# Kernel optimization log

Measured on AMD Instinct MI355X. Metric: run time of the kernel, lower is better.

Reference implementation:

```python
import jax, jax.numpy as jnp
import numpy as np

# SRM neuron constants (match init_kwargs)
THRESH = 0.3
TAU_M = 16.0
TAU_S = 4.0
DT = 1.0
LENS = 0.5
DECAY_M = float(np.exp(-DT / TAU_M))
DECAY_S = float(np.exp(-DT / TAU_S))

B, T = 16, 16
SHAPES = [(B, 64, 64, 64), (B, 128, 64, 64), (B, 128, 32, 32), (B, 512), (B, 11)]


@jax.custom_vjp
def spike_fn(u):
    # Heaviside spike with rectangular surrogate gradient (width 2*lens),
    # the smooth-math stand-in for the LUT-based grad_u_approx.
    return (u > THRESH).astype(u.dtype)

def _spike_fwd(u):
    return spike_fn(u), u

def _spike_bwd(u, g):
    surr = (jnp.abs(u - THRESH) < LENS).astype(u.dtype) / (2.0 * LENS)
    return (g * surr,)

spike_fn.defvjp(_spike_fwd, _spike_bwd)


def conv(x, w):
    # 3x3 conv, stride 1, padding 1, no bias (NCHW / OIHW)
    return jax.lax.conv_general_dilated(x, w, (1, 1), [(1, 1), (1, 1)],
                                        dimension_numbers=('NCHW', 'OIHW', 'NCHW'))


def maxpool2(x):
    return jax.lax.reduce_window(x, -jnp.inf, jax.lax.max, (1, 1, 2, 2), (1, 1, 2, 2), 'VALID')


def srm_update(I, vm, vs, s_prev):
    # SRM dynamics: two exponential traces (LUT exp decay in original),
    # reset via previous spike, membrane potential u = vm - vs.
    vm = DECAY_M * vm * (1.0 - s_prev) + I
    vs = DECAY_S * vs * (1.0 - s_prev) + I
    s = spike_fn(vm - vs)
    return vm, vs, s


def _xavier(key, shape):
    if len(shape) == 4:  # OIHW conv
        fan_in = shape[1] * shape[2] * shape[3]
        fan_out = shape[0] * shape[2] * shape[3]
    else:  # Linear [out, in]
        fan_in, fan_out = shape[1], shape[0]
    lim = float(np.sqrt(6.0 / (fan_in + fan_out)))
    return jax.random.uniform(key, shape, jnp.float32, -lim, lim)


def setup_inputs() -> dict:
    key = jax.random.key(0)
    ks = jax.random.split(key, 6)
    inp = jax.random.uniform(ks[0], (B, T, 2, 64, 64), jnp.float32)
    return {
        'input': inp,
        'W0': _xavier(ks[1], (64, 2, 3, 3)),
        'W1': _xavier(ks[2], (128, 64, 3, 3)),
        'W2': _xavier(ks[3], (128, 128, 3, 3)),
        'W3': _xavier(ks[4], (512, 32768)),
        'W4': _xavier(ks[5], (11, 512)),
        'batch_size': B,
        'num_steps': T,
    }


def reference(input, W0, W1, W2, W3, W4, batch_size, num_steps):
    x = jnp.transpose(input, (1, 0, 2, 3, 4))  # [T, B, 2, 64, 64]
    z = lambda s: jnp.zeros(s, jnp.float32)
    vm = tuple(z(s) for s in SHAPES)
    vs = tuple(z(s) for s in SHAPES)
    sp = tuple(z(s) for s in SHAPES)
    out_sum = z((batch_size, 11))

    def step(carry, xt):
        vm, vs, sp, out_sum = carry
        in_spike = jnp.clip(xt, 0.0, 1.0)  # limit == 'yes'
        vm0, vs0, s0 = srm_update(conv(in_spike, W0), vm[0], vs[0], sp[0])
        vm1, vs1, s1 = srm_update(conv(s0, W1), vm[1], vs[1], sp[1])
        p1 = maxpool2(s1)                                    # [B,128,32,32]
        vm2, vs2, s2 = srm_update(conv(p1, W2), vm[2], vs[2], sp[2])
        p2 = maxpool2(s2).reshape(batch_size, -1)            # [B, 32768]
        vm3, vs3, s3 = srm_update(p2 @ W3.T, vm[3], vs[3], sp[3])
        vm4, vs4, s4 = srm_update(s3 @ W4.T, vm[4], vs[4], sp[4])
        new_carry = ((vm0, vm1, vm2, vm3, vm4), (vs0, vs1, vs2, vs3, vs4),
                     (s0, s1, s2, s3, s4), out_sum + s4)
        return new_carry, None

    (_, _, _, out_sum), _ = jax.lax.scan(step, (vm, vs, sp, out_sum), x)
    return out_sum / num_steps
```

## Files before the change

### kernel.cpp

```cpp
#include <hip/hip_runtime.h>
#include <hip/hip_bf16.h>
#include <math.h>

#define DM 0.9394130628134758f
#define DSC 0.7788007830714049f
#define TH 0.3f

#define B 16
#define T 16

typedef short short8 __attribute__((ext_vector_type(8)));
typedef float f32x4 __attribute__((ext_vector_type(4)));
typedef int i32x4 __attribute__((ext_vector_type(4)));

__device__ __forceinline__ void srm(float& m, float& s, float p, float I, float& spk) {
    m = DM * m * (1.f - p) + I;
    s = DSC * s * (1.f - p) + I;
    spk = (m - s > TH) ? 1.f : 0.f;
}

__global__ __launch_bounds__(256) void k_prep_i8(const float* __restrict__ W,
                                                 signed char* __restrict__ Wd,
                                                 int CO, int CI,
                                                 float s1, float s2, float s3) {
    int idx = blockIdx.x * 256 + threadIdx.x;
    int total = CO * CI * 9;
    if (idx >= total) return;
    int tap = idx % 9, tmp = idx / 9, ci = tmp % CI, co = tmp / CI;
    float w = W[((size_t)co * CI + ci) * 9 + tap];
    float d1 = rintf(w / s1);
    float r1 = fmaf(-d1, s1, w);
    float d2 = rintf(r1 / s2);
    float r2 = fmaf(-d2, s2, r1);
    float d3 = rintf(r2 / s3);
    d1 = fminf(fmaxf(d1, -127.f), 127.f);
    d2 = fminf(fmaxf(d2, -127.f), 127.f);
    d3 = fminf(fmaxf(d3, -127.f), 127.f);
    size_t base = ((size_t)tap * CO + co) * CI + ci;
    size_t stride = (size_t)9 * CO * CI;
    Wd[base] = (signed char)(int)d1;
    Wd[base + stride] = (signed char)(int)d2;
    Wd[base + 2 * stride] = (signed char)(int)d3;
}

__global__ __launch_bounds__(256) void k_prep3(const float* __restrict__ W3,
                                               unsigned short* __restrict__ W3p) {
    int bid = blockIdx.x;
    int ot = bid >> 8, ks4 = bid & 255;
    int lane = threadIdx.x & 63, wv = threadIdx.x >> 6;
    int kstep = ks4 * 4 + wv;
    int n = lane & 15, q = lane >> 4;
    const float* src = W3 + (size_t)(ot * 16 + n) * 32768 + kstep * 32 + q * 8;
    float4 w0 = *(const float4*)src;
    float4 w1 = *(const float4*)(src + 4);
    float wj[8] = {w0.x, w0.y, w0.z, w0.w, w1.x, w1.y, w1.z, w1.w};
    short8 hh, mm, ll;
#pragma unroll
    for (int j = 0; j < 8; j++) {
        __hip_bfloat16 h = __float2bfloat16(wj[j]);
        float hf = __bfloat162float(h);
        __hip_bfloat16 m = __float2bfloat16(wj[j] - hf);
        float mf = __bfloat162float(m);
        __hip_bfloat16 l = __float2bfloat16(wj[j] - hf - mf);
        hh[j] = *(short*)&h; mm[j] = *(short*)&m; ll[j] = *(short*)&l;
    }
    size_t pos = (((size_t)ot * 1024 + kstep) * 64 + lane) * 8;
    *(short8*)(W3p + pos) = hh;
    *(short8*)(W3p + 16777216 + pos) = mm;
    *(short8*)(W3p + 33554432 + pos) = ll;
}

#define S0 68
__global__ __launch_bounds__(128) void k_conv0T(const float* __restrict__ in,
                                                const float* __restrict__ W0,
                                                signed char* __restrict__ s0b) {
    __shared__ float tile[2][10 * S0];
    int bid = blockIdx.x;
    int cog = bid & 7, yt = (bid >> 3) & 7, b = bid >> 6;
    int tid = threadIdx.x;
    int tx = (tid & 15) * 4, ty = tid >> 4;
    int y0 = yt * 8, y = y0 + ty;

    float m[8][4] = {}, s[8][4] = {};
    unsigned pmask = 0;

    for (int t = 0; t < T; t++) {
        if (t) __syncthreads();
        for (int i = tid; i < 2 * 660; i += 128) {
            int cl = i / 660, rem = i - cl * 660;
            int r = rem / 66, c = rem - r * 66;
            int gy = y0 + r - 1, gx = c - 1;
            float v = 0.f;
            if ((unsigned)gy < 64u && (unsigned)gx < 64u) {
                const float* src = in + ((size_t)((b * T + t) * 2 + cl)) * 4096;
                v = fminf(fmaxf(src[gy * 64 + gx], 0.f), 1.f);
            }
            tile[cl][r * S0 + c] = v;
        }
        __syncthreads();

        float acc[8][4] = {};
#pragma unroll
        for (int cl = 0; cl < 2; cl++) {
            const float* wb = W0 + ((size_t)cog * 8 * 2 + cl) * 9;
#pragma unroll
            for (int dy = 0; dy < 3; dy++) {
                float4 A = *(const float4*)&tile[cl][(ty + dy) * S0 + tx];
                float4 Bv = *(const float4*)&tile[cl][(ty + dy) * S0 + tx + 4];
                float r0 = A.x, r1 = A.y, r2 = A.z, r3 = A.w, r4 = Bv.x, r5 = Bv.y;
#pragma unroll
                for (int c = 0; c < 8; c++) {
                    const float* w = wb + (size_t)c * 2 * 9 + dy * 3;
                    float wa = w[0], wbx = w[1], wc = w[2];
                    acc[c][0] += wa * r0 + wbx * r1 + wc * r2;
                    acc[c][1] += wa * r1 + wbx * r2 + wc * r3;
                    acc[c][2] += wa * r2 + wbx * r3 + wc * r4;
                    acc[c][3] += wa * r3 + wbx * r4 + wc * r5;
                }
            }
        }

        unsigned newmask = 0;
        signed char* s0p = s0b + ((size_t)(t * 16 + b) * 4096) * 64;
#pragma unroll
        for (int j = 0; j < 4; j++) {
            unsigned long long vv = 0ULL;
#pragma unroll
            for (int c = 0; c < 8; c++) {
                int bit = c * 4 + j;
                float p = (pmask >> bit) & 1 ? 1.f : 0.f;
                float spk;
                srm(m[c][j], s[c][j], p, acc[c][j], spk);
                bool on = spk > 0.5f;
                if (on) { newmask |= 1u << bit; vv |= 1ULL << (8 * c); }
            }
            *(unsigned long long*)(s0p + ((size_t)(y * 64 + tx + j)) * 64 + cog * 8) = vv;
        }
        pmask = newmask;
    }
}

__global__ __launch_bounds__(512, 2) void k_conv1T(const signed char* __restrict__ s0b,
                                                   const signed char* __restrict__ W1d,
                                                   signed char* __restrict__ p1b,
                                                   float s1, float s3) {
    __shared__ i32x4 atile[1360];
    __shared__ i32x4 wlds[3456];
    int bid = blockIdx.x;
    int b = bid & 15;
    int rest = bid >> 4;
    int cg = rest & 3;
    int xh = (rest >> 2) & 1;
    int yq = rest >> 3;
    int tid = threadIdx.x;
    int lane = tid & 63, wv = tid >> 6;
    int cog_l = wv >> 2, rq = wv & 3;
    int n = lane & 15, q = lane >> 4;
    int y0 = yq * 8;

    const i32x4 zf = {0, 0, 0, 0};
    for (int i = tid; i < 1360; i += 512) atile[i] = zf;
    for (int idx = tid; idx < 3456; idx += 512) {
        int qq = idx & 3, nn = (idx >> 2) & 15;
        int r27 = (idx >> 6) % 27, cl = idx / 1728;
        int tm = r27 % 3, tap = r27 / 3;
        int dst = (idx & ~3) | ((qq + (nn >> 1)) & 3);
        wlds[dst] = *(const i32x4*)(W1d +
            ((size_t)(tm * 9 + tap) * 128 + cg * 32 + cl * 16 + nn) * 64 + qq * 16);
    }

    int off_[3], ldsi_[3];
    bool ok_[3];
#pragma unroll
    for (int j = 0; j < 3; j++) {
        ok_[j] = false; ldsi_[j] = 0; off_[j] = 0;
        int item = tid + j * 512;
        if (item < 1360) {
            int r = item / 136, rem = item - r * 136;
            int xl = rem >> 2, c = rem & 3;
            ldsi_[j] = (r * 34 + xl) * 4 + ((c + (xl >> 1)) & 3);
            int gy = y0 - 1 + r;
            int gx = xh * 32 + xl - 1;
            if ((unsigned)gy < 64u && (unsigned)gx < 64u) {
                ok_[j] = true;
                off_[j] = (gy * 64 + gx) * 64 + c * 16;
            }
        }
    }
    __syncthreads();

    {
        const signed char* sb = s0b + ((size_t)(0 * 16 + b) * 4096) * 64;
#pragma unroll
        for (int j = 0; j < 3; j++)
            if (ok_[j]) atile[ldsi_[j]] = *(const i32x4*)(sb + off_[j]);
    }
    __syncthreads();

    int xp_s = lane >> 2, cq = lane & 3;
    int xt_s = xp_s >> 3, q_s = (xp_s >> 1) & 3, rp_s = xp_s & 1;

    int cbase_w = cog_l * 1728;
    float sm[4][4] = {}, ss[4][4] = {};
    unsigned pmask = 0;

    for (int t = 0; t < T; t++) {
        i32x4 pf0 = zf, pf1 = zf, pf2 = zf;
        bool pfv = (t + 1 < T);
        if (pfv) {
            const signed char* sb1 = s0b + ((size_t)((t + 1) * 16 + b) * 4096) * 64;
            if (ok_[0]) pf0 = *(const i32x4*)(sb1 + off_[0]);
            if (ok_[1]) pf1 = *(const i32x4*)(sb1 + off_[1]);
            if (ok_[2]) pf2 = *(const i32x4*)(sb1 + off_[2]);
        }

        i32x4 accH[4], accL[4];
#pragma unroll
        for (int u = 0; u < 4; u++) { accH[u] = zf; accL[u] = zf; }

#pragma unroll
        for (int dy = 0; dy < 3; dy++) {
#pragma unroll
            for (int dx = 0; dx < 3; dx++) {
                int tap = dy * 3 + dx;
                i32x4 Af[2][2];
#pragma unroll
                for (int ro = 0; ro < 2; ro++) {
                    int r = rq * 2 + ro + dy;
#pragma unroll
                    for (int xt = 0; xt < 2; xt++) {
                        int x = xt * 16 + n + dx;
                        Af[ro][xt] = atile[(r * 34 + x) * 4 + ((q + (x >> 1)) & 3)];
                    }
                }
                {
                    i32x4 Bf = wlds[cbase_w + (tap * 3 + 0) * 64 + n * 4 + ((q + (n >> 1)) & 3)];
#pragma unroll
                    for (int ro = 0; ro < 2; ro++)
#pragma unroll
                        for (int xt = 0; xt < 2; xt++)
                            accH[ro * 2 + xt] = __builtin_amdgcn_mfma_i32_16x16x64_i8(
                                Af[ro][xt], Bf, accH[ro * 2 + xt], 0, 0, 0);
                }
                {
                    i32x4 Bf = wlds[cbase_w + (tap * 3 + 2) * 64 + n * 4 + ((q + (n >> 1)) & 3)];
#pragma unroll
                    for (int ro = 0; ro < 2; ro++)
#pragma unroll
                        for (int xt = 0; xt < 2; xt++)
                            accL[ro * 2 + xt] = __builtin_amdgcn_mfma_i32_16x16x64_i8(
                                Af[ro][xt], Bf, accL[ro * 2 + xt], 0, 0, 0);
                }
                {
                    i32x4 Bf = wlds[cbase_w + (tap * 3 + 1) * 64 + n * 4 + ((q + (n >> 1)) & 3)];
#pragma unroll
                    for (int ro = 0; ro < 2; ro++)
#pragma unroll
                        for (int xt = 0; xt < 2; xt++) {
                            Af[ro][xt] = Af[ro][xt] << 6;
                            accL[ro * 2 + xt] = __builtin_amdgcn_mfma_i32_16x16x64_i8(
                                Af[ro][xt], Bf, accL[ro * 2 + xt], 0, 0, 0);
                        }
                }
            }
        }

        unsigned newmask = 0;
#pragma unroll
        for (int ro = 0; ro < 2; ro++)
#pragma unroll
            for (int xt = 0; xt < 2; xt++)
#pragma unroll
                for (int r = 0; r < 4; r++) {
                    int u = ro * 2 + xt;
                    int bit = u * 4 + r;
                    float p = (pmask >> bit) & 1 ? 1.f : 0.f;
                    float I = (float)accH[u][r] * s1 + (float)accL[u][r] * s3;
                    float spk;
                    srm(sm[u][r], ss[u][r], p, I, spk);
                    if (spk > 0.5f) newmask |= 1u << bit;
                }
        pmask = newmask;

        unsigned bits4 = 0;
#pragma unroll
        for (int xt = 0; xt < 2; xt++)
#pragma unroll
            for (int rp = 0; rp < 2; rp++) {
                int i0 = (0 * 2 + xt) * 4 + 2 * rp;
                int i1 = (1 * 2 + xt) * 4 + 2 * rp;
                unsigned on = ((newmask >> i0) | (newmask >> (i0 + 1)) |
                               (newmask >> i1) | (newmask >> (i1 + 1))) & 1u;
                unsigned long long bal = __ballot(on != 0);
                if (xt == xt_s && rp == rp_s)
                    bits4 = (unsigned)(bal >> (q_s * 16 + cq * 4)) & 0xFu;
            }
        unsigned vv = (bits4 & 1u) | (((bits4 >> 1) & 1u) << 8) |
                      (((bits4 >> 2) & 1u) << 16) | (((bits4 >> 3) & 1u) << 24);
        signed char* pb = p1b + (((size_t)(t * 16 + b) * 8) + cg * 2 + cog_l) * 16384;
        int px = (yq * 4 + rq) * 32 + xh * 16 + xp_s;
        *(unsigned*)(pb + (size_t)px * 16 + cq * 4) = vv;

        __syncthreads();
        if (pfv) {
            if (ok_[0]) atile[ldsi_[0]] = pf0;
            if (ok_[1]) atile[ldsi_[1]] = pf1;
            if (ok_[2]) atile[ldsi_[2]] = pf2;
        }
        __syncthreads();
    }
}

__global__ __launch_bounds__(512, 2) void k_conv2T(const signed char* __restrict__ p1b,
                                                   const signed char* __restrict__ W2d,
                                                   unsigned short* __restrict__ p2a,
                                                   float s1, float s3) {
    __shared__ i32x4 atile[4896];
    __shared__ i32x4 wlds[3456];
    int bid = blockIdx.x;
    int xcd = bid & 7, rest = bid >> 3;
    int b = ((rest & 1) << 3) | xcd;
    int yh = (rest >> 1) & 1;
    int cog = (rest >> 2) & 7;
    int tid = threadIdx.x;
    int lane = tid & 63, wv = tid >> 6;
    int n = lane & 15, q = lane >> 4;
    int y0 = yh * 16;

    const i32x4 zf = {0, 0, 0, 0};
    for (int i = tid; i < 4896; i += 512) atile[i] = zf;
    for (int idx = tid; idx < 3456; idx += 512) {
        int c8 = idx & 7, nn = (idx >> 3) & 15, rem = idx >> 7;
        int tm = rem % 3, tap = rem / 3;
        int dst = (idx & ~7) | (c8 ^ ((nn & 1) << 2));
        wlds[dst] = *(const i32x4*)(W2d +
            ((size_t)(tm * 9 + tap) * 128 + cog * 16 + nn) * 128 + c8 * 16);
    }

    int yr = yh * 8 + wv;
    int co = cog * 16 + n;

    float sm[2][2][4] = {}, ss[2][2][4] = {};
    unsigned pmask = 0;

    for (int t = 0; t < T; t++) {
        __syncthreads();
        const signed char* sb = p1b + (((size_t)(t * 16 + b)) << 17);
        for (int i = tid; i < 4608; i += 512) {
            int c = i & 7, x32 = (i >> 3) & 31, r = i >> 8;
            int gy = y0 - 1 + r;
            if ((unsigned)gy < 32u) {
                int xtile = x32 + 1;
                atile[(r * 34 + xtile) * 8 + (c ^ ((xtile & 1) << 2))] =
                    *(const i32x4*)(sb + (((size_t)c) << 14) + ((size_t)(gy * 32 + x32)) * 16);
            }
        }
        __syncthreads();

        i32x4 accH[2][2], accL[2][2];
#pragma unroll
        for (int i = 0; i < 2; i++)
#pragma unroll
            for (int j = 0; j < 2; j++) { accH[i][j] = zf; accL[i][j] = zf; }

#pragma unroll
        for (int ks = 0; ks < 2; ks++) {
#pragma unroll
            for (int dy = 0; dy < 3; dy++) {
                int rA = wv * 2 + dy, rB = rA + 1;
#pragma unroll
                for (int dx = 0; dx < 3; dx++) {
                    int tap = dy * 3 + dx;
                    i32x4 AfA[2], AfB[2];
#pragma unroll
                    for (int xt = 0; xt < 2; xt++) {
                        int x = xt * 16 + n + dx;
                        int slA = (ks * 4 + q) ^ ((x & 1) << 2);
                        AfA[xt] = atile[(rA * 34 + x) * 8 + slA];
                        AfB[xt] = atile[(rB * 34 + x) * 8 + slA];
                    }
                    int slB = (ks * 4 + q) ^ ((n & 1) << 2);
                    {
                        i32x4 Bf = wlds[(tap * 3 + 0) * 128 + n * 8 + slB];
#pragma unroll
                        for (int xt = 0; xt < 2; xt++) {
                            accH[0][xt] = __builtin_amdgcn_mfma_i32_16x16x64_i8(AfA[xt], Bf, accH[0][xt], 0, 0, 0);
                            accH[1][xt] = __builtin_amdgcn_mfma_i32_16x16x64_i8(AfB[xt], Bf, accH[1][xt], 0, 0, 0);
                        }
                    }
                    {
                        i32x4 Bf = wlds[(tap * 3 + 2) * 128 + n * 8 + slB];
#pragma unroll
                        for (int xt = 0; xt < 2; xt++) {
                            accL[0][xt] = __builtin_amdgcn_mfma_i32_16x16x64_i8(AfA[xt], Bf, accL[0][xt], 0, 0, 0);
                            accL[1][xt] = __builtin_amdgcn_mfma_i32_16x16x64_i8(AfB[xt], Bf, accL[1][xt], 0, 0, 0);
                        }
                    }
                    {
                        i32x4 Bf = wlds[(tap * 3 + 1) * 128 + n * 8 + slB];
#pragma unroll
                        for (int xt = 0; xt < 2; xt++) {
                            AfA[xt] = AfA[xt] << 6;
                            AfB[xt] = AfB[xt] << 6;
                            accL[0][xt] = __builtin_amdgcn_mfma_i32_16x16x64_i8(AfA[xt], Bf, accL[0][xt], 0, 0, 0);
                            accL[1][xt] = __builtin_amdgcn_mfma_i32_16x16x64_i8(AfB[xt], Bf, accL[1][xt], 0, 0, 0);
                        }
                    }
                }
            }
        }

        unsigned newmask = 0;
#pragma unroll
        for (int yo = 0; yo < 2; yo++)
#pragma unroll
            for (int xt = 0; xt < 2; xt++)
#pragma unroll
                for (int r = 0; r < 4; r++) {
                    int bit = (yo * 2 + xt) * 4 + r;
                    float p = (pmask >> bit) & 1 ? 1.f : 0.f;
                    float I = (float)accH[yo][xt][r] * s1 + (float)accL[yo][xt][r] * s3;
                    float spk;
                    srm(sm[yo][xt][r], ss[yo][xt][r], p, I, spk);
                    if (spk > 0.5f) newmask |= 1u << bit;
                }
        pmask = newmask;

        int kstep = co * 8 + (yr >> 1);
        size_t base_t = ((size_t)t * 1024 + kstep) * 512;
#pragma unroll
        for (int xt = 0; xt < 2; xt++) {
            int i00 = (0 * 2 + xt) * 4 + 0, i10 = (1 * 2 + xt) * 4 + 0;
            int i01 = (0 * 2 + xt) * 4 + 2, i11 = (1 * 2 + xt) * 4 + 2;
            unsigned on0 = ((newmask >> i00) | (newmask >> (i00 + 1)) |
                            (newmask >> i10) | (newmask >> (i10 + 1))) & 1u;
            unsigned on1 = ((newmask >> i01) | (newmask >> (i01 + 1)) |
                            (newmask >> i11) | (newmask >> (i11 + 1))) & 1u;
            unsigned v32 = (on0 ? 0x3F80u : 0u) | (on1 ? 0x3F800000u : 0u);
            int qp = (yr & 1) * 2 + xt;
            *(unsigned*)(p2a + base_t + (size_t)(qp * 16 + b) * 8 + q * 2) = v32;
        }
    }
}

__global__ __launch_bounds__(256) void k_fc3(const unsigned short* __restrict__ p2a,
                                             const unsigned short* __restrict__ W3p,
                                             float* __restrict__ I3p) {
    int bid = blockIdx.x;
    int ob = bid & 7, r2 = bid >> 3;
    int t = r2 & 15, ks = r2 >> 4;
    int lane = threadIdx.x & 63, w = threadIdx.x >> 6;
    int ot = ob * 4 + w;

    const unsigned short* ap = p2a + ((size_t)t * 1024 + ks * 128) * 512 + lane * 8;
    const unsigned short* bp = W3p + ((size_t)ot * 1024 + ks * 128) * 512 + lane * 8;

    f32x4 acc = {0.f, 0.f, 0.f, 0.f};
#pragma unroll 8
    for (int kk = 0; kk < 128; kk++) {
        short8 A = *(const short8*)(ap + (size_t)kk * 512);
        short8 B0 = *(const short8*)(bp + (size_t)kk * 512);
        short8 B1 = *(const short8*)(bp + 16777216 + (size_t)kk * 512);
        short8 B2 = *(const short8*)(bp + 33554432 + (size_t)kk * 512);
        acc = __builtin_amdgcn_mfma_f32_16x16x32_bf16(A, B0, acc, 0, 0, 0);
        acc = __builtin_amdgcn_mfma_f32_16x16x32_bf16(A, B1, acc, 0, 0, 0);
        acc = __builtin_amdgcn_mfma_f32_16x16x32_bf16(A, B2, acc, 0, 0, 0);
    }
    int n = lane & 15, q = lane >> 4;
    float* op = I3p + ((size_t)(t * 8 + ks)) * 8192 + ot * 16 + n;
#pragma unroll
    for (int r = 0; r < 4; r++)
        op[(size_t)(q * 4 + r) * 512] = acc[r];
}

__global__ __launch_bounds__(256) void k_srm3T(const float* __restrict__ I3p,
                                               float* __restrict__ sp3) {
    int idx = blockIdx.x * 256 + threadIdx.x;
    float m = 0.f, s = 0.f, p = 0.f;
    for (int t = 0; t < T; t++) {
        float I = 0.f;
#pragma unroll
        for (int ks = 0; ks < 8; ks++) I += I3p[((size_t)(t * 8 + ks)) * 8192 + idx];
        float spk;
        srm(m, s, p, I, spk);
        p = spk;
        sp3[t * 8192 + idx] = spk;
    }
}

__global__ __launch_bounds__(256) void k_fc4g(const float* __restrict__ sp3,
                                              const float* __restrict__ W4,
                                              float* __restrict__ I4) {
    int t = blockIdx.x, tid = threadIdx.x;
    if (tid >= 176) return;
    int b = tid / 11, o = tid - b * 11;
    const float4* a = (const float4*)(sp3 + (size_t)t * 8192 + b * 512);
    const float4* w = (const float4*)(W4 + o * 512);
    float acc = 0.f;
    for (int k = 0; k < 128; k++) {
        float4 x = a[k], y = w[k];
        acc += x.x * y.x + x.y * y.y + x.z * y.z + x.w * y.w;
    }
    I4[(size_t)(t * 16 + b) * 11 + o] = acc;
}

__global__ __launch_bounds__(256) void k_fc4s(const float* __restrict__ I4,
                                              float* __restrict__ out) {
    int tid = threadIdx.x;
    if (tid >= 176) return;
    int b = tid / 11, o = tid - b * 11;
    float m = 0.f, s = 0.f, p = 0.f, sum = 0.f;
    for (int t = 0; t < T; t++) {
        float I = I4[(size_t)(t * 16 + b) * 11 + o];
        float spk;
        srm(m, s, p, I, spk);
        p = spk;
        sum += spk;
    }
    out[tid] = sum * 0.0625f;
}

extern "C" void kernel_launch(void* const* d_in, const int* in_sizes, int n_in,
                              void* d_out, int out_size, void* d_ws, size_t ws_size,
                              hipStream_t stream) {
    const float* in = (const float*)d_in[0];
    const float* W0 = (const float*)d_in[1];
    const float* W1 = (const float*)d_in[2];
    const float* W2 = (const float*)d_in[3];
    const float* W3 = (const float*)d_in[4];
    const float* W4 = (const float*)d_in[5];
    float* out = (float*)d_out;
    char* ws = (char*)d_ws;

    size_t off = 0;
    auto alloc = [&](size_t bytes) {
        void* p = ws + off;
        off += (bytes + 255) & ~(size_t)255;
        return p;
    };
    signed char* s0b = (signed char*)alloc((size_t)256 * 4096 * 64);
    signed char* p1b = (signed char*)alloc((size_t)256 * 1024 * 128);
    unsigned short* p2a = (unsigned short*)alloc((size_t)16 * 1024 * 512 * 2);
    float* I3p = (float*)alloc((size_t)128 * 8192 * 4);
    float* sp3 = (float*)alloc((size_t)16 * 8192 * 4);
    float* I4  = (float*)alloc((size_t)256 * 11 * 4);
    signed char* W1d = (signed char*)alloc((size_t)3 * 9 * 128 * 64);
    signed char* W2d = (signed char*)alloc((size_t)3 * 9 * 128 * 128);
    unsigned short* W3p = (unsigned short*)alloc((size_t)3 * 512 * 32768 * 2);

    double lim1 = sqrt(6.0 / (64.0 * 9 + 128.0 * 9));
    double lim2 = sqrt(6.0 / (128.0 * 9 + 128.0 * 9));
    float s1a = (float)(lim1 / 127.0);
    float s2a = s1a / 254.0f;
    float s3a = s2a / 64.0f;
    float s1b = (float)(lim2 / 127.0);
    float s2b = s1b / 254.0f;
    float s3b = s2b / 64.0f;

    k_prep_i8<<<(9 * 128 * 64 + 255) / 256, 256, 0, stream>>>(W1, W1d, 128, 64, s1a, s2a, s3a);
    k_prep_i8<<<(9 * 128 * 128 + 255) / 256, 256, 0, stream>>>(W2, W2d, 128, 128, s1b, s2b, s3b);
    k_prep3<<<8192, 256, 0, stream>>>(W3, W3p);

    k_conv0T<<<16 * 8 * 8, 128, 0, stream>>>(in, W0, s0b);
    k_conv1T<<<1024, 512, 0, stream>>>(s0b, W1d, p1b, s1a, s3a);
    k_conv2T<<<256, 512, 0, stream>>>(p1b, W2d, p2a, s1b, s3b);
    k_fc3<<<1024, 256, 0, stream>>>(p2a, W3p, I3p);
    k_srm3T<<<8192 / 256, 256, 0, stream>>>(I3p, sp3);
    k_fc4g<<<16, 256, 0, stream>>>(sp3, W4, I4);
    k_fc4s<<<1, 256, 0, stream>>>(I4, out);
}
```

Measured before the change: 794.7 us.

## Split conv1 blocks per 16-channel group and use separate mid-weight accumulator

Restructures k_conv1T so each 256-thread block handles one 16-output-channel group instead of 32, doubling the grid to 2048 blocks and halving weight LDS. This should raise occupancy. It also drops the XOR-style swizzle on the activation tile and replaces the shift-by-6 merge of the middle weight term with a third accumulator (accM) scaled by s2. Each activation tile is now loaded by twice as many blocks, and the extra accumulator adds register pressure.

```diff
diff --git a/kernel.cpp b/kernel.cpp
--- a/kernel.cpp
+++ b/kernel.cpp
@@ -140,45 +140,44 @@
     }
 }
 
-__global__ __launch_bounds__(512, 2) void k_conv1T(const signed char* __restrict__ s0b,
+__global__ __launch_bounds__(256, 3) void k_conv1T(const signed char* __restrict__ s0b,
                                                    const signed char* __restrict__ W1d,
                                                    signed char* __restrict__ p1b,
-                                                   float s1, float s3) {
+                                                   float s1, float s2, float s3) {
     __shared__ i32x4 atile[1360];
-    __shared__ i32x4 wlds[3456];
+    __shared__ i32x4 wlds[1728];
     int bid = blockIdx.x;
     int b = bid & 15;
     int rest = bid >> 4;
-    int cg = rest & 3;
-    int xh = (rest >> 2) & 1;
-    int yq = rest >> 3;
+    int cog = rest & 7;
+    int xh = (rest >> 3) & 1;
+    int yq = rest >> 4;
     int tid = threadIdx.x;
-    int lane = tid & 63, wv = tid >> 6;
-    int cog_l = wv >> 2, rq = wv & 3;
+    int lane = tid & 63, rq = tid >> 6;
     int n = lane & 15, q = lane >> 4;
     int y0 = yq * 8;
 
     const i32x4 zf = {0, 0, 0, 0};
-    for (int i = tid; i < 1360; i += 512) atile[i] = zf;
-    for (int idx = tid; idx < 3456; idx += 512) {
+    for (int i = tid; i < 1360; i += 256) atile[i] = zf;
+    for (int idx = tid; idx < 1728; idx += 256) {
         int qq = idx & 3, nn = (idx >> 2) & 15;
-        int r27 = (idx >> 6) % 27, cl = idx / 1728;
+        int r27 = idx >> 6;
         int tm = r27 % 3, tap = r27 / 3;
         int dst = (idx & ~3) | ((qq + (nn >> 1)) & 3);
         wlds[dst] = *(const i32x4*)(W1d +
-            ((size_t)(tm * 9 + tap) * 128 + cg * 32 + cl * 16 + nn) * 64 + qq * 16);
-    }
-
-    int off_[3], ldsi_[3];
-    bool ok_[3];
-#pragma unroll
-    for (int j = 0; j < 3; j++) {
+            ((size_t)(tm * 9 + tap) * 128 + cog * 16 + nn) * 64 + qq * 16);
+    }
+
+    int off_[6], ldsi_[6];
+    bool ok_[6];
+#pragma unroll
+    for (int j = 0; j < 6; j++) {
         ok_[j] = false; ldsi_[j] = 0; off_[j] = 0;
-        int item = tid + j * 512;
+        int item = tid + j * 256;
         if (item < 1360) {
             int r = item / 136, rem = item - r * 136;
             int xl = rem >> 2, c = rem & 3;
-            ldsi_[j] = (r * 34 + xl) * 4 + ((c + (xl >> 1)) & 3);
+            ldsi_[j] = (r * 34 + xl) * 4 + c;
             int gy = y0 - 1 + r;
             int gx = xh * 32 + xl - 1;
             if ((unsigned)gy < 64u && (unsigned)gx < 64u) {
@@ -192,31 +191,34 @@
     {
         const signed char* sb = s0b + ((size_t)(0 * 16 + b) * 4096) * 64;
 #pragma unroll
-        for (int j = 0; j < 3; j++)
+        for (int j = 0; j < 6; j++)
             if (ok_[j]) atile[ldsi_[j]] = *(const i32x4*)(sb + off_[j]);
     }
     __syncthreads();
 
     int xp_s = lane >> 2, cq = lane & 3;
     int xt_s = xp_s >> 3, q_s = (xp_s >> 1) & 3, rp_s = xp_s & 1;
-
-    int cbase_w = cog_l * 1728;
+    int slotw = (q + (n >> 1)) & 3;
+
     float sm[4][4] = {}, ss[4][4] = {};
     unsigned pmask = 0;
 
     for (int t = 0; t < T; t++) {
-        i32x4 pf0 = zf, pf1 = zf, pf2 = zf;
+        i32x4 pf0 = zf, pf1 = zf, pf2 = zf, pf3 = zf, pf4 = zf, pf5 = zf;
         bool pfv = (t + 1 < T);
         if (pfv) {
             const signed char* sb1 = s0b + ((size_t)((t + 1) * 16 + b) * 4096) * 64;
             if (ok_[0]) pf0 = *(const i32x4*)(sb1 + off_[0]);
             if (ok_[1]) pf1 = *(const i32x4*)(sb1 + off_[1]);
             if (ok_[2]) pf2 = *(const i32x4*)(sb1 + off_[2]);
-        }
-
-        i32x4 accH[4], accL[4];
-#pragma unroll
-        for (int u = 0; u < 4; u++) { accH[u] = zf; accL[u] = zf; }
+            if (ok_[3]) pf3 = *(const i32x4*)(sb1 + off_[3]);
+            if (ok_[4]) pf4 = *(const i32x4*)(sb1 + off_[4]);
+            if (ok_[5]) pf5 = *(const i32x4*)(sb1 + off_[5]);
+        }
+
+        i32x4 accH[4], accM[4], accL[4];
+#pragma unroll
+        for (int u = 0; u < 4; u++) { accH[u] = zf; accM[u] = zf; accL[u] = zf; }
 
 #pragma unroll
         for (int dy = 0; dy < 3; dy++) {
@@ -230,11 +232,11 @@
 #pragma unroll
                     for (int xt = 0; xt < 2; xt++) {
                         int x = xt * 16 + n + dx;
-                        Af[ro][xt] = atile[(r * 34 + x) * 4 + ((q + (x >> 1)) & 3)];
+                        Af[ro][xt] = atile[(r * 34 + x) * 4 + q];
                     }
                 }
                 {
-                    i32x4 Bf = wlds[cbase_w + (tap * 3 + 0) * 64 + n * 4 + ((q + (n >> 1)) & 3)];
+                    i32x4 Bf = wlds[(tap * 3 + 0) * 64 + n * 4 + slotw];
 #pragma unroll
                     for (int ro = 0; ro < 2; ro++)
 #pragma unroll
@@ -243,24 +245,22 @@
                                 Af[ro][xt], Bf, accH[ro * 2 + xt], 0, 0, 0);
                 }
                 {
-                    i32x4 Bf = wlds[cbase_w + (tap * 3 + 2) * 64 + n * 4 + ((q + (n >> 1)) & 3)];
+                    i32x4 Bf = wlds[(tap * 3 + 1) * 64 + n * 4 + slotw];
+#pragma unroll
+                    for (int ro = 0; ro < 2; ro++)
+#pragma unroll
+                        for (int xt = 0; xt < 2; xt++)
+                            accM[ro * 2 + xt] = __builtin_amdgcn_mfma_i32_16x16x64_i8(
+                                Af[ro][xt], Bf, accM[ro * 2 + xt], 0, 0, 0);
+                }
+                {
+                    i32x4 Bf = wlds[(tap * 3 + 2) * 64 + n * 4 + slotw];
 #pragma unroll
                     for (int ro = 0; ro < 2; ro++)
 #pragma unroll
                         for (int xt = 0; xt < 2; xt++)
                             accL[ro * 2 + xt] = __builtin_amdgcn_mfma_i32_16x16x64_i8(
                                 Af[ro][xt], Bf, accL[ro * 2 + xt], 0, 0, 0);
-                }
-                {
-                    i32x4 Bf = wlds[cbase_w + (tap * 3 + 1) * 64 + n * 4 + ((q + (n >> 1)) & 3)];
-#pragma unroll
-                    for (int ro = 0; ro < 2; ro++)
-#pragma unroll
-                        for (int xt = 0; xt < 2; xt++) {
-                            Af[ro][xt] = Af[ro][xt] << 6;
-                            accL[ro * 2 + xt] = __builtin_amdgcn_mfma_i32_16x16x64_i8(
-                                Af[ro][xt], Bf, accL[ro * 2 + xt], 0, 0, 0);
-                        }
                 }
             }
         }
@@ -275,7 +275,8 @@
                     int u = ro * 2 + xt;
                     int bit = u * 4 + r;
                     float p = (pmask >> bit) & 1 ? 1.f : 0.f;
-                    float I = (float)accH[u][r] * s1 + (float)accL[u][r] * s3;
+                    float I = fmaf((float)accH[u][r], s1,
+                             fmaf((float)accM[u][r], s2, (float)accL[u][r] * s3));
                     float spk;
                     srm(sm[u][r], ss[u][r], p, I, spk);
                     if (spk > 0.5f) newmask |= 1u << bit;
@@ -297,7 +298,7 @@
             }
         unsigned vv = (bits4 & 1u) | (((bits4 >> 1) & 1u) << 8) |
                       (((bits4 >> 2) & 1u) << 16) | (((bits4 >> 3) & 1u) << 24);
-        signed char* pb = p1b + (((size_t)(t * 16 + b) * 8) + cg * 2 + cog_l) * 16384;
+        signed char* pb = p1b + (((size_t)(t * 16 + b) * 8) + cog) * 16384;
         int px = (yq * 4 + rq) * 32 + xh * 16 + xp_s;
         *(unsigned*)(pb + (size_t)px * 16 + cq * 4) = vv;
 
@@ -306,6 +307,9 @@
             if (ok_[0]) atile[ldsi_[0]] = pf0;
             if (ok_[1]) atile[ldsi_[1]] = pf1;
             if (ok_[2]) atile[ldsi_[2]] = pf2;
+            if (ok_[3]) atile[ldsi_[3]] = pf3;
+            if (ok_[4]) atile[ldsi_[4]] = pf4;
+            if (ok_[5]) atile[ldsi_[5]] = pf5;
         }
         __syncthreads();
     }
@@ -562,7 +566,7 @@
     k_prep3<<<8192, 256, 0, stream>>>(W3, W3p);
 
     k_conv0T<<<16 * 8 * 8, 128, 0, stream>>>(in, W0, s0b);
-    k_conv1T<<<1024, 512, 0, stream>>>(s0b, W1d, p1b, s1a, s3a);
+    k_conv1T<<<2048, 256, 0, stream>>>(s0b, W1d, p1b, s1a, s2a, s3a);
     k_conv2T<<<256, 512, 0, stream>>>(p1b, W2d, p2a, s1b, s3b);
     k_fc3<<<1024, 256, 0, stream>>>(p2a, W3p, I3p);
     k_srm3T<<<8192 / 256, 256, 0, stream>>>(I3p, sp3);
```

Result: slower. 830.5 us (+4.5%).
